# Optimization experiments

Measured on AMD Instinct MI355X. Metric: run time of the kernel, lower is better.

The kernel has to match this reference:

```python
import jax, jax.numpy as jnp
import numpy as np

# dims
B, S, T = 64, 128, 64            # batch, src_len, tgt_len
H, E, V = 1024, 512, 16000       # hidden, embedding, vocab
ENC = 2 * H                      # bidirectional encoder dim
SOS = 1
SCALE = 0.02


def setup_inputs() -> dict:
    key = jax.random.key(0)
    ks = jax.random.split(key, 13)
    n = lambda k, sh: jax.random.normal(k, sh, dtype=jnp.float32) * SCALE
    return {
        "encoder_outputs": jax.random.normal(ks[0], (B, S, ENC), dtype=jnp.float32),
        "encoder_hidden": jax.random.normal(ks[1], (1, B, H), dtype=jnp.float32),
        "target": jax.random.randint(ks[2], (B, T), 0, V, dtype=jnp.int64),
        "emb": n(ks[3], (V, E)),                 # embedding table
        "Wa": n(ks[4], (H, H + ENC)),            # attn Linear weight ([query | enc] -> H)
        "ba": jnp.zeros((H,), jnp.float32),
        "v": n(ks[5], (H,)),                     # attn score vector (no bias)
        "W_ih": n(ks[6], (3 * H, E + ENC)),      # GRU input weights (r,z,n)
        "b_ih": jnp.zeros((3 * H,), jnp.float32),
        "W_hh": n(ks[7], (3 * H, H)),            # GRU hidden weights
        "b_hh": jnp.zeros((3 * H,), jnp.float32),
        "Wo": n(ks[8], (V, H)),                  # output projection
        "bo": jnp.zeros((V,), jnp.float32),
    }


def reference(encoder_outputs, encoder_hidden, target, emb, Wa, ba, v,
              W_ih, b_ih, W_hh, b_hh, Wo, bo):
    h0 = encoder_hidden[0]                                   # [B,H] (num_layers=1)
    # teacher_forcing_p=1.0 -> decoder input is SOS then target[:, :-1]
    tokens = jnp.concatenate(
        [jnp.full((B, 1), SOS, dtype=target.dtype), target[:, :-1]], axis=1)  # [B,T]

    # attn Linear acts on concat([query, enc_out]); split weight accordingly
    Wa_q, Wa_e = Wa[:, :H], Wa[:, H:]
    # encoder part is time-invariant -> precompute once: [B,S,H]
    enc_proj = jnp.einsum('bse,he->bsh', encoder_outputs, Wa_e)

    def step(h, tok):
        x_emb = emb[tok]                                     # [B,E]
        q = h @ Wa_q.T + ba                                  # [B,H]
        energy = jnp.tanh(q[:, None, :] + enc_proj)          # [B,S,H]
        scores = energy @ v                                  # [B,S]
        alpha = jax.nn.softmax(scores, axis=1)               # [B,S]
        ctx = jnp.einsum('bs,bsd->bd', alpha, encoder_outputs)  # [B,ENC]
        x = jnp.concatenate([x_emb, ctx], axis=1)            # [B,E+ENC]
        # torch GRU cell
        gi = x @ W_ih.T + b_ih                               # [B,3H]
        gh = h @ W_hh.T + b_hh
        ir, iz, inn = jnp.split(gi, 3, axis=1)
        hr, hz, hn = jnp.split(gh, 3, axis=1)
        r = jax.nn.sigmoid(ir + hr)
        z = jax.nn.sigmoid(iz + hz)
        n = jnp.tanh(inn + r * hn)
        h_new = (1.0 - z) * n + z * h                        # [B,H]
        out = h_new @ Wo.T + bo                              # [B,V]
        return h_new, out

    _, outs = jax.lax.scan(step, h0, tokens.T)               # [T,B,V]
    return jnp.transpose(outs, (1, 0, 2))                    # [B,T,V]
```

## Files before the change

kernel.cpp:

```cpp
#include <hip/hip_runtime.h>
#include <hip/hip_bf16.h>

#define B_   64
#define S_   128
#define T_   64
#define H_   1024
#define E_   512
#define V_   16000
#define ENC_ 2048
#define XDIM_ (E_ + ENC_)
#define G3_  (3 * H_)
#define QGH_ (4 * H_)
#define NB_  256

#define SMEM_ENCP   0
#define SMEM_SCR    65536
#define SMEM_TOTAL  102400

typedef __attribute__((ext_vector_type(8))) short bf16x8;
typedef __attribute__((ext_vector_type(8))) unsigned short u16x8;
typedef __attribute__((ext_vector_type(4))) float f32x4;

__device__ __forceinline__ ushort f2bf(float x) {
    __hip_bfloat16 h = __float2bfloat16(x);
    return *reinterpret_cast<ushort*>(&h);
}
__device__ __forceinline__ float bf2f(ushort u) {
    return __uint_as_float((unsigned)u << 16);
}
__device__ __forceinline__ float sigmoidf_(float x) {
    return 1.f / (1.f + expf(-x));
}

template <typename T>
__device__ __forceinline__ void atstore(T* p, T v) {
    __hip_atomic_store(p, v, __ATOMIC_RELAXED, __HIP_MEMORY_SCOPE_AGENT);
}

__device__ __forceinline__ void gload_lds16(const ushort* g, ushort* l) {
    __builtin_amdgcn_global_load_lds(
        (const __attribute__((address_space(1))) unsigned int*)g,
        (__attribute__((address_space(3))) unsigned int*)l, 16, 0, 0);
}

__device__ __forceinline__ void pollge(const unsigned* f, unsigned v) {
    while (__hip_atomic_load(f, __ATOMIC_RELAXED, __HIP_MEMORY_SCOPE_AGENT) < v)
        __builtin_amdgcn_s_sleep(1);
}
__device__ __forceinline__ void sigrel(unsigned* f, unsigned v) {
    __hip_atomic_store(f, v, __ATOMIC_RELAXED, __HIP_MEMORY_SCOPE_AGENT);
}

__global__ __launch_bounds__(256) void gemm128_bf16(
    const ushort* __restrict__ A, int lda,
    const ushort* __restrict__ W, int ldw,
    const float* __restrict__ bias,
    float* __restrict__ Cf, ushort* __restrict__ Cb, int ldc,
    int K)
{
    const int bn0 = blockIdx.x * 128;
    const int bm0 = blockIdx.y * 128;
    const int tid = threadIdx.x;
    const int wv  = tid >> 6;
    const int lane = tid & 63;

    __shared__ ushort As[128 * 32];
    __shared__ ushort Bs[128 * 32];

    const int srow = tid >> 2;
    const int scol = (tid & 3) * 8;

    const ushort* gA0 = A + (size_t)(bm0 + srow) * lda + scol;
    const ushort* gA1 = gA0 + (size_t)64 * lda;
    const ushort* gB0 = W + (size_t)(bn0 + srow) * ldw + scol;
    const ushort* gB1 = gB0 + (size_t)64 * ldw;

    ushort* lA0 = &As[tid * 8];
    ushort* lA1 = &As[2048 + tid * 8];
    ushort* lB0 = &Bs[tid * 8];
    ushort* lB1 = &Bs[2048 + tid * 8];

    const int wr0 = (wv >> 1) * 64;
    const int wc0 = (wv & 1) * 64;
    const int frow = lane & 15;
    const int fk   = (lane >> 4) * 8;

    f32x4 acc[4][4];
#pragma unroll
    for (int i = 0; i < 4; ++i)
#pragma unroll
        for (int j = 0; j < 4; ++j) acc[i][j] = (f32x4){0.f, 0.f, 0.f, 0.f};

    for (int k0 = 0; k0 < K; k0 += 32) {
        gload_lds16(gA0 + k0, lA0);
        gload_lds16(gA1 + k0, lA1);
        gload_lds16(gB0 + k0, lB0);
        gload_lds16(gB1 + k0, lB1);
        __syncthreads();

        bf16x8 af[4], bf[4];
#pragma unroll
        for (int rb = 0; rb < 4; ++rb)
            af[rb] = *reinterpret_cast<const bf16x8*>(&As[(wr0 + rb * 16 + frow) * 32 + fk]);
#pragma unroll
        for (int cb = 0; cb < 4; ++cb)
            bf[cb] = *reinterpret_cast<const bf16x8*>(&Bs[(wc0 + cb * 16 + frow) * 32 + fk]);
#pragma unroll
        for (int rb = 0; rb < 4; ++rb)
#pragma unroll
            for (int cb = 0; cb < 4; ++cb)
                acc[rb][cb] = __builtin_amdgcn_mfma_f32_16x16x32_bf16(af[rb], bf[cb], acc[rb][cb], 0, 0, 0);
        __syncthreads();
    }

    const int quad = lane >> 4;
#pragma unroll
    for (int cb = 0; cb < 4; ++cb) {
        const int col = bn0 + wc0 + cb * 16 + frow;
        const float bv = bias ? bias[col] : 0.f;
#pragma unroll
        for (int rb = 0; rb < 4; ++rb) {
            const int row0 = bm0 + wr0 + rb * 16 + quad * 4;
            f32x4 a = acc[rb][cb];
#pragma unroll
            for (int r = 0; r < 4; ++r) {
                const float val = a[r] + bv;
                if (Cb) Cb[(size_t)(row0 + r) * ldc + col] = f2bf(val);
                else    Cf[(size_t)(row0 + r) * ldc + col] = val;
            }
        }
    }
}

__global__ __launch_bounds__(256) void pack_bf16(
    const float* __restrict__ src, int src_ld, int c0, int ncols,
    ushort* __restrict__ dst, size_t total)
{
    size_t i = (size_t)blockIdx.x * 256 + threadIdx.x;
    const size_t stride = (size_t)gridDim.x * 256;
    for (; i < total; i += stride) {
        size_t r = i / (size_t)ncols;
        int c = (int)(i - r * (size_t)ncols);
        dst[i] = f2bf(src[r * (size_t)src_ld + c0 + c]);
    }
}

__global__ __launch_bounds__(256) void gather_emb(
    const int* __restrict__ target, const float* __restrict__ emb,
    ushort* __restrict__ dst)
{
    const int row = blockIdx.x;
    const int b = row >> 6;
    const int t = row & 63;
    const int tok = (t == 0) ? 1 : target[b * T_ + t - 1];
    const float* e = emb + (size_t)tok * E_;
    ushort* d = dst + (size_t)row * E_;
    for (int c = threadIdx.x; c < E_; c += 256) d[c] = f2bf(e[c]);
}

__global__ __launch_bounds__(256) void pack_bhq(
    const float* __restrict__ ba, const float* __restrict__ bhh,
    float* __restrict__ dst)
{
    const int j = blockIdx.x * 256 + threadIdx.x;
    if (j < H_) dst[j] = ba[j];
    else if (j < QGH_) dst[j] = bhh[j - H_];
}

__global__ __launch_bounds__(256) void barinit(unsigned* f) {
    const int i = blockIdx.x * 256 + threadIdx.x;
    if (i < 32768) f[i] = 0u;
}

__global__ __launch_bounds__(512) void decoder_persist(
    const ushort* __restrict__ encp,
    const ushort* __restrict__ enc,
    const ushort* __restrict__ ench,
    const float*  __restrict__ ench_f,
    const ushort* __restrict__ Whq,
    const ushort* __restrict__ Wie,
    const float*  __restrict__ bhq,
    const float*  __restrict__ vvec,
    const float*  __restrict__ giemb,
    float* __restrict__ q_all,
    float* __restrict__ scores_all,
    ushort* __restrict__ ctx_all,
    float* __restrict__ hall_f,
    ushort* __restrict__ hall_b,
    unsigned* __restrict__ aflag,
    unsigned* __restrict__ sflag,
    unsigned* __restrict__ xflag,
    unsigned* __restrict__ hflag)
{
    extern __shared__ __align__(16) char smem[];
    const int blk = blockIdx.x;
    const int tid = threadIdx.x;
    const int wv = tid >> 6;
    const int lane = tid & 63;
    const int frow = lane & 15;
    const int fk = (lane >> 4) * 8;

    const int ab = blk >> 2;
    const int aq = blk & 3;
    const int qbg = blk >> 6;
    const int qc0 = (blk & 63) * 16;
    const int jt = blk >> 2;
    const int cb0 = (blk & 3) * 16;

    {
        const char* src = (const char*)(encp + ((size_t)ab * S_ + aq * 32) * H_);
#pragma unroll
        for (int r = 0; r < 8; ++r) {
            const int ci = r * 8 + wv;
            gload_lds16((const ushort*)(src + ci * 1024 + lane * 16),
                        (ushort*)(smem + SMEM_ENCP + ci * 1024 + lane * 16));
        }
    }
    float vr[16];
    *reinterpret_cast<f32x4*>(&vr[0])  = *reinterpret_cast<const f32x4*>(vvec + lane * 8);
    *reinterpret_cast<f32x4*>(&vr[4])  = *reinterpret_cast<const f32x4*>(vvec + lane * 8 + 4);
    *reinterpret_cast<f32x4*>(&vr[8])  = *reinterpret_cast<const f32x4*>(vvec + 512 + lane * 8);
    *reinterpret_cast<f32x4*>(&vr[12]) = *reinterpret_cast<const f32x4*>(vvec + 512 + lane * 8 + 4);
    __syncthreads();

    for (int t = 0; t < T_; ++t) {
        const ushort* hb = t ? (hall_b + (size_t)(t - 1) * H_) : ench;
        const float*  hf = t ? (hall_f + (size_t)(t - 1) * H_) : ench_f;
        const int ldh = t ? (T_ * H_) : H_;
        float* q = q_all + (size_t)t * B_ * H_;
        float* scores = scores_all + (size_t)t * B_ * S_;
        ushort* ctx = ctx_all + (size_t)t * B_ * ENC_;

        if (t) {
            if (tid < 64) pollge(&hflag[(tid * 4 + qbg) * 32], (unsigned)t);
            __syncthreads();
        }

        {
            f32x4 (*red)[64] = reinterpret_cast<f32x4(*)[64]>(smem + SMEM_SCR);
            const ushort* Arow = hb + (size_t)(qbg * 16 + frow) * ldh + wv * 128 + fk;
            const ushort* Brow = Whq + (size_t)(qc0 + frow) * H_ + wv * 128 + fk;
            f32x4 acc = (f32x4){0.f, 0.f, 0.f, 0.f};
#pragma unroll
            for (int c = 0; c < 4; ++c) {
                bf16x8 a = *reinterpret_cast<const bf16x8*>(Arow + c * 32);
                bf16x8 b = *reinterpret_cast<const bf16x8*>(Brow + c * 32);
                acc = __builtin_amdgcn_mfma_f32_16x16x32_bf16(a, b, acc, 0, 0, 0);
            }
            red[wv][lane] = acc;
            __syncthreads();
            if (wv == 0) {
                f32x4 s = red[0][lane];
#pragma unroll
                for (int w = 1; w < 8; ++w) s += red[w][lane];
                const int col = qc0 + frow;
                const float bv = bhq[col];
                const int b0 = qbg * 16 + (lane >> 4) * 4;
#pragma unroll
                for (int r = 0; r < 4; ++r)
                    atstore(&q[(size_t)(b0 + r) * H_ + col], s[r] + bv);
            }
        }
        __syncthreads();
        if (tid == 0) sigrel(&aflag[blk * 32], (unsigned)(t + 1));

        if (tid < 64) pollge(&aflag[((ab >> 4) * 64 + tid) * 32], (unsigned)(t + 1));
        __syncthreads();

        {
            float qr[16];
            const float* qrow = q + (size_t)ab * H_;
            *reinterpret_cast<f32x4*>(&qr[0])  = *reinterpret_cast<const f32x4*>(qrow + lane * 8);
            *reinterpret_cast<f32x4*>(&qr[4])  = *reinterpret_cast<const f32x4*>(qrow + lane * 8 + 4);
            *reinterpret_cast<f32x4*>(&qr[8])  = *reinterpret_cast<const f32x4*>(qrow + 512 + lane * 8);
            *reinterpret_cast<f32x4*>(&qr[12]) = *reinterpret_cast<const f32x4*>(qrow + 512 + lane * 8 + 4);
#pragma unroll
            for (int i = 0; i < 4; ++i) {
                const int sl = wv * 4 + i;
                const char* rowp = smem + SMEM_ENCP + sl * 2048;
                u16x8 e0 = *reinterpret_cast<const u16x8*>(rowp + lane * 16);
                u16x8 e1 = *reinterpret_cast<const u16x8*>(rowp + 1024 + lane * 16);
                float p = 0.f;
#pragma unroll
                for (int j = 0; j < 8; ++j)
                    p += vr[j] * tanhf(qr[j] + bf2f(e0[j]));
#pragma unroll
                for (int j = 0; j < 8; ++j)
                    p += vr[8 + j] * tanhf(qr[8 + j] + bf2f(e1[j]));
#pragma unroll
                for (int off = 32; off; off >>= 1) p += __shfl_xor(p, off);
                if (lane == 0) atstore(&scores[ab * S_ + aq * 32 + sl], p);
            }
            __syncthreads();
            if (tid == 0) sigrel(&sflag[blk * 32], (unsigned)(t + 1));

            const int e0c = aq * 512;
            const ushort* ebase = enc + (size_t)ab * S_ * ENC_ + e0c + lane * 8;
            u16x8 epre[16];
#pragma unroll
            for (int i = 0; i < 16; ++i)
                epre[i] = *reinterpret_cast<const u16x8*>(ebase + (size_t)(wv + i * 8) * ENC_);

            if (tid < 4) pollge(&sflag[(ab * 4 + tid) * 32], (unsigned)(t + 1));
            __syncthreads();

            float* part = reinterpret_cast<float*>(smem + SMEM_SCR);
            float* al   = reinterpret_cast<float*>(smem + SMEM_SCR + 16384);
            if (tid < 64) {
                float a0 = scores[ab * S_ + tid];
                float a1 = scores[ab * S_ + tid + 64];
                float m = fmaxf(a0, a1);
#pragma unroll
                for (int off = 32; off; off >>= 1) m = fmaxf(m, __shfl_xor(m, off));
                float e0v = expf(a0 - m), e1v = expf(a1 - m);
                float ssum = e0v + e1v;
#pragma unroll
                for (int off = 32; off; off >>= 1) ssum += __shfl_xor(ssum, off);
                const float inv = 1.f / ssum;
                al[tid] = e0v * inv;
                al[tid + 64] = e1v * inv;
            }
            __syncthreads();
            float acc[8];
#pragma unroll
            for (int j = 0; j < 8; ++j) acc[j] = 0.f;
#pragma unroll
            for (int i = 0; i < 16; ++i) {
                u16x8 ev = epre[i];
                const float a = al[wv + i * 8];
#pragma unroll
                for (int j = 0; j < 8; ++j)
                    acc[j] = fmaf(a, bf2f(ev[j]), acc[j]);
            }
            *reinterpret_cast<f32x4*>(part + wv * 512 + lane * 8)     = *reinterpret_cast<f32x4*>(&acc[0]);
            *reinterpret_cast<f32x4*>(part + wv * 512 + lane * 8 + 4) = *reinterpret_cast<f32x4*>(&acc[4]);
            __syncthreads();
            float scol = part[tid];
#pragma unroll
            for (int w = 1; w < 8; ++w) scol += part[w * 512 + tid];
            atstore(&ctx[(size_t)ab * ENC_ + e0c + tid], f2bf(scol));
        }
        __syncthreads();
        if (tid == 0) sigrel(&xflag[blk * 32], (unsigned)(t + 1));

        if (tid < 64) pollge(&xflag[(cb0 * 4 + tid) * 32], (unsigned)(t + 1));
        __syncthreads();

        {
            f32x4 (*redp)[4][64] = reinterpret_cast<f32x4(*)[4][64]>(smem + SMEM_SCR);
            float (*gt)[16][16] = reinterpret_cast<float(*)[16][16]>(smem + SMEM_SCR + 32768);
            const int j0 = jt * 16;

            f32x4 a0 = (f32x4){0.f, 0.f, 0.f, 0.f};
            f32x4 a1 = a0;
            f32x4 a2 = a0;
            f32x4 a3 = a0;

            {
                const ushort* Ar = hb + (size_t)(cb0 + frow) * ldh + wv * 128 + fk;
                const ushort* Br = Whq + (size_t)(1024 + j0 + frow) * H_ + wv * 128 + fk;
                const ushort* Bz = Br + (size_t)1024 * H_;
                const ushort* Bn = Br + (size_t)2048 * H_;
#pragma unroll
                for (int c = 0; c < 4; ++c) {
                    bf16x8 av = *reinterpret_cast<const bf16x8*>(Ar + c * 32);
                    a0 = __builtin_amdgcn_mfma_f32_16x16x32_bf16(av, *reinterpret_cast<const bf16x8*>(Br + c * 32), a0, 0, 0, 0);
                    a1 = __builtin_amdgcn_mfma_f32_16x16x32_bf16(av, *reinterpret_cast<const bf16x8*>(Bz + c * 32), a1, 0, 0, 0);
                    a3 = __builtin_amdgcn_mfma_f32_16x16x32_bf16(av, *reinterpret_cast<const bf16x8*>(Bn + c * 32), a3, 0, 0, 0);
                }
            }
            {
                const ushort* Ar = ctx + (size_t)(cb0 + frow) * ENC_ + wv * 256 + fk;
                const ushort* Br = Wie + (size_t)(j0 + frow) * ENC_ + wv * 256 + fk;
                const ushort* Bz = Br + (size_t)1024 * ENC_;
                const ushort* Bn = Br + (size_t)2048 * ENC_;
#pragma unroll
                for (int c = 0; c < 8; ++c) {
                    bf16x8 av = *reinterpret_cast<const bf16x8*>(Ar + c * 32);
                    a0 = __builtin_amdgcn_mfma_f32_16x16x32_bf16(av, *reinterpret_cast<const bf16x8*>(Br + c * 32), a0, 0, 0, 0);
                    a1 = __builtin_amdgcn_mfma_f32_16x16x32_bf16(av, *reinterpret_cast<const bf16x8*>(Bz + c * 32), a1, 0, 0, 0);
                    a2 = __builtin_amdgcn_mfma_f32_16x16x32_bf16(av, *reinterpret_cast<const bf16x8*>(Bn + c * 32), a2, 0, 0, 0);
                }
            }
            redp[wv][0][lane] = a0;
            redp[wv][1][lane] = a1;
            redp[wv][2][lane] = a2;
            redp[wv][3][lane] = a3;
            __syncthreads();
            if (wv < 4) {
                f32x4 s = redp[0][wv][lane];
#pragma unroll
                for (int w = 1; w < 8; ++w) s += redp[w][wv][lane];
                const int row0 = (lane >> 4) * 4;
#pragma unroll
                for (int r = 0; r < 4; ++r) gt[wv][row0 + r][frow] = s[r];
            }
            __syncthreads();
            if (tid < 256) {
                const int bl = tid >> 4, jl = tid & 15;
                const int b = cb0 + bl;
                const int j = j0 + jl;
                const size_t gr = (size_t)(b * T_ + t) * G3_;
                const float rsum = gt[0][bl][jl] + giemb[gr + j]          + bhq[1024 + j];
                const float zsum = gt[1][bl][jl] + giemb[gr + H_ + j]     + bhq[2048 + j];
                const float inn  = gt[2][bl][jl] + giemb[gr + 2 * H_ + j];
                const float hn   = gt[3][bl][jl] + bhq[3072 + j];
                const float r = sigmoidf_(rsum);
                const float z = sigmoidf_(zsum);
                const float n = tanhf(inn + r * hn);
                const float hnew = (1.f - z) * n + z * hf[(size_t)b * ldh + j];
                const size_t ho = (size_t)b * (T_ * H_) + (size_t)t * H_ + j;
                atstore(&hall_f[ho], hnew);
                atstore(&hall_b[ho], f2bf(hnew));
            }
        }
        __syncthreads();
        if (tid == 0) sigrel(&hflag[blk * 32], (unsigned)(t + 1));
    }
}

static inline int pgrid(size_t total) {
    size_t nb = (total + 255) / 256;
    if (nb > 4096) nb = 4096;
    return (int)nb;
}

extern "C" void kernel_launch(void* const* d_in, const int* in_sizes, int n_in,
                              void* d_out, int out_size, void* d_ws, size_t ws_size,
                              hipStream_t stream) {
    const float* enc    = (const float*)d_in[0];
    const float* enc_h  = (const float*)d_in[1];
    const int*   target = (const int*)  d_in[2];
    const float* emb    = (const float*)d_in[3];
    const float* Wa     = (const float*)d_in[4];
    const float* ba     = (const float*)d_in[5];
    const float* vvec   = (const float*)d_in[6];
    const float* W_ih   = (const float*)d_in[7];
    const float* b_ih   = (const float*)d_in[8];
    const float* W_hh   = (const float*)d_in[9];
    const float* b_hh   = (const float*)d_in[10];
    const float* Wo     = (const float*)d_in[11];
    const float* bo     = (const float*)d_in[12];
    float* out = (float*)d_out;

    char* p = (char*)d_ws;
    auto alloc_u16 = [&](size_t n) { ushort* r = (ushort*)p; p += n * 2; return r; };
    auto alloc_f32 = [&](size_t n) { float* r = (float*)p; p += n * 4; return r; };

    ushort* enc_bf  = alloc_u16((size_t)B_ * S_ * ENC_);
    ushort* encp_bf = alloc_u16((size_t)B_ * S_ * H_);
    ushort* Wo_bf   = alloc_u16((size_t)V_ * H_);
    ushort* Wae_bf  = alloc_u16((size_t)H_ * ENC_);
    ushort* Whq_bf  = alloc_u16((size_t)QGH_ * H_);
    ushort* Wie_bf  = alloc_u16((size_t)G3_ * ENC_);
    ushort* Wiee_bf = alloc_u16((size_t)G3_ * E_);
    ushort* ench_bf = alloc_u16((size_t)B_ * H_);
    ushort* Xemb_bf = alloc_u16((size_t)B_ * T_ * E_);
    ushort* hall_bf = alloc_u16((size_t)B_ * T_ * H_);
    ushort* ctx_all = alloc_u16((size_t)T_ * B_ * ENC_);
    float* hall_f   = alloc_f32((size_t)B_ * T_ * H_);
    float* giemb    = alloc_f32((size_t)B_ * T_ * G3_);
    float* q_all    = alloc_f32((size_t)T_ * B_ * H_);
    float* scr_all  = alloc_f32((size_t)T_ * B_ * S_);
    float* bhq      = alloc_f32((size_t)QGH_);
    unsigned* flags = (unsigned*)alloc_f32(33024);
    unsigned* aflag = flags;
    unsigned* sflag = flags + 8192;
    unsigned* xflag = flags + 16384;
    unsigned* hflag = flags + 24576;

    const int LDW = H_ + ENC_;

    pack_bf16<<<pgrid((size_t)B_*S_*ENC_), 256, 0, stream>>>(enc, ENC_, 0, ENC_, enc_bf, (size_t)B_*S_*ENC_);
    pack_bf16<<<pgrid((size_t)V_*H_), 256, 0, stream>>>(Wo, H_, 0, H_, Wo_bf, (size_t)V_*H_);
    pack_bf16<<<pgrid((size_t)H_*ENC_), 256, 0, stream>>>(Wa, LDW, H_, ENC_, Wae_bf, (size_t)H_*ENC_);
    pack_bf16<<<pgrid((size_t)H_*H_), 256, 0, stream>>>(Wa, LDW, 0, H_, Whq_bf, (size_t)H_*H_);
    pack_bf16<<<pgrid((size_t)G3_*H_), 256, 0, stream>>>(W_hh, H_, 0, H_, Whq_bf + (size_t)H_*H_, (size_t)G3_*H_);
    pack_bf16<<<pgrid((size_t)G3_*ENC_), 256, 0, stream>>>(W_ih, XDIM_, E_, ENC_, Wie_bf, (size_t)G3_*ENC_);
    pack_bf16<<<pgrid((size_t)G3_*E_), 256, 0, stream>>>(W_ih, XDIM_, 0, E_, Wiee_bf, (size_t)G3_*E_);
    pack_bf16<<<pgrid((size_t)B_*H_), 256, 0, stream>>>(enc_h, H_, 0, H_, ench_bf, (size_t)B_*H_);
    gather_emb<<<B_*T_, 256, 0, stream>>>(target, emb, Xemb_bf);
    pack_bhq<<<QGH_/256, 256, 0, stream>>>(ba, b_hh, bhq);
    barinit<<<128, 256, 0, stream>>>(flags);

    gemm128_bf16<<<dim3(H_/128, (B_*S_)/128), 256, 0, stream>>>(
        enc_bf, ENC_, Wae_bf, ENC_, nullptr, nullptr, encp_bf, H_, ENC_);
    gemm128_bf16<<<dim3(G3_/128, (B_*T_)/128), 256, 0, stream>>>(
        Xemb_bf, E_, Wiee_bf, E_, b_ih, giemb, nullptr, G3_, E_);

    decoder_persist<<<NB_, 512, SMEM_TOTAL, stream>>>(
        encp_bf, enc_bf, ench_bf, enc_h, Whq_bf, Wie_bf, bhq, vvec, giemb,
        q_all, scr_all, ctx_all, hall_f, hall_bf, aflag, sflag, xflag, hflag);

    gemm128_bf16<<<dim3(V_/128, (B_*T_)/128), 256, 0, stream>>>(
        hall_bf, H_, Wo_bf, H_, bo, out, nullptr, V_, H_);
}
```

Before: 2.834 ms.

## Fuse output projection into persistent decoder, overlapping with next timestep

Drops the separate final vocab-projection GEMM. The persistent decoder kernel now computes each timestep's output logits (h_t @ Wo^T + bo) itself, one step late, after all blocks have published h_t. Each of 250 blocks handles 64 vocab columns using direct global-load MFMAs, with the aim of hiding the projection inside the latency-bound recurrent loop. The cost is an extra all-block poll per step, which adds sync latency on the critical path. Each block also rereads 64x1024 of Wo from L2/HBM every step with no LDS reuse.

```diff
diff --git a/kernel.cpp b/kernel.cpp
--- a/kernel.cpp
+++ b/kernel.cpp
@@ -12,6 +12,7 @@
 #define G3_  (3 * H_)
 #define QGH_ (4 * H_)
 #define NB_  256
+#define NDB_ 250
 
 #define SMEM_ENCP   0
 #define SMEM_SCR    65536
@@ -179,6 +180,8 @@
     const float*  __restrict__ ench_f,
     const ushort* __restrict__ Whq,
     const ushort* __restrict__ Wie,
+    const ushort* __restrict__ Wob,
+    const float*  __restrict__ bo,
     const float*  __restrict__ bhq,
     const float*  __restrict__ vvec,
     const float*  __restrict__ giemb,
@@ -187,6 +190,7 @@
     ushort* __restrict__ ctx_all,
     float* __restrict__ hall_f,
     ushort* __restrict__ hall_b,
+    float* __restrict__ out,
     unsigned* __restrict__ aflag,
     unsigned* __restrict__ sflag,
     unsigned* __restrict__ xflag,
@@ -206,6 +210,36 @@
     const int qc0 = (blk & 63) * 16;
     const int jt = blk >> 2;
     const int cb0 = (blk & 3) * 16;
+
+    auto dphase = [&](int tD) {
+        const int n0 = blk * 64;
+        const int mt = wv >> 1;
+        const int ntp = (wv & 1) * 2;
+        const ushort* Arow = hall_b + ((size_t)(mt * 16 + frow) * T_ + tD) * H_ + fk;
+        const ushort* Br0 = Wob + (size_t)(n0 + ntp * 16 + frow) * H_ + fk;
+        const ushort* Br1 = Br0 + (size_t)16 * H_;
+        f32x4 o0 = (f32x4){0.f, 0.f, 0.f, 0.f}, o1 = o0;
+#pragma unroll 8
+        for (int c = 0; c < 32; ++c) {
+            bf16x8 av = *reinterpret_cast<const bf16x8*>(Arow + c * 32);
+            o0 = __builtin_amdgcn_mfma_f32_16x16x32_bf16(
+                av, *reinterpret_cast<const bf16x8*>(Br0 + c * 32), o0, 0, 0, 0);
+            o1 = __builtin_amdgcn_mfma_f32_16x16x32_bf16(
+                av, *reinterpret_cast<const bf16x8*>(Br1 + c * 32), o1, 0, 0, 0);
+        }
+        const int quad = lane >> 4;
+        const int col0 = n0 + ntp * 16 + frow;
+        const int col1 = col0 + 16;
+        const float bv0 = bo[col0];
+        const float bv1 = bo[col1];
+#pragma unroll
+        for (int r = 0; r < 4; ++r) {
+            const int b = mt * 16 + quad * 4 + r;
+            float* orow = out + ((size_t)b * T_ + tD) * V_;
+            orow[col0] = o0[r] + bv0;
+            orow[col1] = o1[r] + bv1;
+        }
+    };
 
     {
         const char* src = (const char*)(encp + ((size_t)ab * S_ + aq * 32) * H_);
@@ -416,6 +450,18 @@
         }
         __syncthreads();
         if (tid == 0) sigrel(&hflag[blk * 32], (unsigned)(t + 1));
+
+        if (t && blk < NDB_) {
+            if (tid < 256) pollge(&hflag[tid * 32], (unsigned)t);
+            __syncthreads();
+            dphase(t - 1);
+        }
+    }
+
+    if (blk < NDB_) {
+        if (tid < 256) pollge(&hflag[tid * 32], (unsigned)T_);
+        __syncthreads();
+        dphase(T_ - 1);
     }
 }
 
@@ -489,9 +535,7 @@
         Xemb_bf, E_, Wiee_bf, E_, b_ih, giemb, nullptr, G3_, E_);
 
     decoder_persist<<<NB_, 512, SMEM_TOTAL, stream>>>(
-        encp_bf, enc_bf, ench_bf, enc_h, Whq_bf, Wie_bf, bhq, vvec, giemb,
-        q_all, scr_all, ctx_all, hall_f, hall_bf, aflag, sflag, xflag, hflag);
-
-    gemm128_bf16<<<dim3(V_/128, (B_*T_)/128), 256, 0, stream>>>(
-        hall_bf, H_, Wo_bf, H_, bo, out, nullptr, V_, H_);
-}
+        encp_bf, enc_bf, ench_bf, enc_h, Whq_bf, Wie_bf, Wo_bf, bo, bhq, vvec,
+        giemb, q_all, scr_all, ctx_all, hall_f, hall_bf, out,
+        aflag, sflag, xflag, hflag);
+}
```

After: 4.230 ms. 1.49x slower.
